# Kernel optimization log

Hardware: AMD Instinct MI355X
Metric: run time of the kernel (lower is better)

The kernel has to match this reference:

```python
import jax, jax.numpy as jnp
import numpy as np

B, T, D = 64, 8192, 128
UNITS = 128

def setup_inputs() -> dict:
    key = jax.random.key(0)
    k1, k2, k3 = jax.random.split(key, 3)
    inputs = jax.random.normal(k1, (B, T, D), dtype=jnp.float32)
    # Dense(units): kernel [D, units], bias [units]
    W_kernel = jax.random.normal(k2, (D, UNITS), dtype=jnp.float32) * (1.0 / np.sqrt(D))
    W_bias = jnp.zeros((UNITS,), dtype=jnp.float32)
    # Dense(1): kernel [units, 1], bias [1]
    V_kernel = jax.random.normal(k3, (UNITS, 1), dtype=jnp.float32) * (1.0 / np.sqrt(UNITS))
    V_bias = jnp.zeros((1,), dtype=jnp.float32)
    return {"inputs": inputs, "W_kernel": W_kernel, "W_bias": W_bias,
            "V_kernel": V_kernel, "V_bias": V_bias}

def reference(inputs, W_kernel, W_bias, V_kernel, V_bias):
    # score: [B, T, units]
    score = jnp.tanh(jnp.einsum('btd,du->btu', inputs, W_kernel) + W_bias)
    # logits: [B, T, 1]; softmax over time axis (axis=1)
    logits = jnp.einsum('btu,uo->bto', score, V_kernel) + V_bias
    attention_weights = jax.nn.softmax(logits, axis=1)
    # weighted sum over time -> [B, D]
    context_vector = jnp.sum(attention_weights * inputs, axis=1)
    return context_vector
```

## Files before the change

### kernel.cpp

```cpp
#include <hip/hip_runtime.h>
#include <hip/hip_bf16.h>

typedef __attribute__((ext_vector_type(8))) short short8;
typedef __attribute__((ext_vector_type(4))) float f32x4;

#define B_SZ 64
#define T_SZ 8192
#define D_SZ 128
#define U_SZ 128
#define T_TILE 64
#define GRID_P 1024
#define TILES_PER_BLK 8
#define P_STRIDE 132
#define WT_LD 136

__device__ __forceinline__ unsigned short f2bf(float f) {
  unsigned int u = __builtin_bit_cast(unsigned int, f);
  u += 0x7fffu + ((u >> 16) & 1u);
  return (unsigned short)(u >> 16);
}

__device__ __forceinline__ float bf2f(unsigned short s) {
  return __builtin_bit_cast(float, (unsigned int)s << 16);
}

__device__ __forceinline__ float fast_tanh(float x) {
  float e = __expf(2.0f * x);
  return 1.0f - 2.0f * __builtin_amdgcn_rcpf(e + 1.0f);
}

template<int CTRL>
__device__ __forceinline__ float dpp_add(float v) {
  int t = __builtin_amdgcn_update_dpp(0, __builtin_bit_cast(int, v),
                                      CTRL, 0xf, 0xf, true);
  return v + __builtin_bit_cast(float, t);
}
__device__ __forceinline__ float row_reduce16(float v) {
  v = dpp_add<0x118>(v);
  v = dpp_add<0x114>(v);
  v = dpp_add<0x112>(v);
  v = dpp_add<0x111>(v);
  return v;
}

__global__ void k_prep(const float* __restrict__ wk, unsigned short* __restrict__ wt) {
  int i = blockIdx.x * 256 + threadIdx.x;
  if (i < D_SZ * U_SZ) {
    int d = i >> 7, u = i & 127;
    wt[u * D_SZ + d] = f2bf(wk[i]);
  }
}

__global__ __launch_bounds__(256) void k_partial(
    const float* __restrict__ x, const unsigned short* __restrict__ wt_g,
    const float* __restrict__ wb, const float* __restrict__ v,
    const float* __restrict__ vb, float* __restrict__ pbuf)
{
  __shared__ unsigned short wt[U_SZ][WT_LD];
  __shared__ float wb_s[U_SZ], v_s[U_SZ];
  __shared__ float logits[T_TILE];
  __shared__ float cpar[4][D_SZ];
  __shared__ float cacc[D_SZ];

  const int tid  = threadIdx.x;
  const int bidx = blockIdx.x;

  for (int i = tid; i < U_SZ * 16; i += 256) {
    int row = i >> 4, c16 = i & 15;
    uint4 val = ((const uint4*)wt_g)[i];
    *(uint4*)&wt[row][c16 * 8] = val;
  }
  if (tid < U_SZ) { wb_s[tid] = wb[tid]; v_s[tid] = v[tid]; cacc[tid] = 0.0f; }
  __syncthreads();

  const int w  = tid >> 6;
  const int l  = tid & 63;
  const int lr = l & 15;
  const int lh = l >> 4;
  const float vbias = vb[0];

  const int b        = bidx >> 4;
  const int row0     = (bidx & 15) * (TILES_PER_BLK * T_TILE);
  const float* xbase = x + ((size_t)b * T_SZ + row0 + w * 16 + lr) * D_SZ + lh * 8;

  float4 pf[8];
#pragma unroll
  for (int kt = 0; kt < 4; ++kt) {
    pf[kt * 2]     = *(const float4*)(xbase + kt * 32);
    pf[kt * 2 + 1] = *(const float4*)(xbase + kt * 32 + 4);
  }
  short8 afrag[4];
#pragma unroll
  for (int kt = 0; kt < 4; ++kt) {
    short8 a;
#pragma unroll
    for (int j = 0; j < 4; ++j) {
      float4 f = pf[kt * 2 + (j >> 1)];
      a[j * 2]     = (short)f2bf(j & 1 ? f.z : f.x);
      a[j * 2 + 1] = (short)f2bf(j & 1 ? f.w : f.y);
    }
    afrag[kt] = a;
  }

  float m_run = -3.0e38f, s_run = 0.0f;

  for (int it = 0; it < TILES_PER_BLK; ++it) {
    if (it + 1 < TILES_PER_BLK) {
      const float* p = xbase + (size_t)(it + 1) * T_TILE * D_SZ;
#pragma unroll
      for (int kt = 0; kt < 4; ++kt) {
        pf[kt * 2]     = *(const float4*)(p + kt * 32);
        pf[kt * 2 + 1] = *(const float4*)(p + kt * 32 + 4);
      }
    }

    float lg[4] = {0.f, 0.f, 0.f, 0.f};
#pragma unroll
    for (int ut = 0; ut < 8; ++ut) {
      f32x4 acc = {0.f, 0.f, 0.f, 0.f};
#pragma unroll
      for (int kt = 0; kt < 4; ++kt) {
        short8 bfrag = *(const short8*)&wt[ut * 16 + lr][kt * 32 + lh * 8];
        acc = __builtin_amdgcn_mfma_f32_16x16x32_bf16(afrag[kt], bfrag, acc, 0, 0, 0);
      }
      const float wbv = wb_s[ut * 16 + lr];
      const float vv  = v_s[ut * 16 + lr];
#pragma unroll
      for (int r = 0; r < 4; ++r)
        lg[r] += fast_tanh(acc[r] + wbv) * vv;
    }
#pragma unroll
    for (int r = 0; r < 4; ++r) lg[r] = row_reduce16(lg[r]);
    if (lr == 15) {
#pragma unroll
      for (int r = 0; r < 4; ++r)
        logits[w * 16 + lh * 4 + r] = lg[r] + vbias;
    }
    __syncthreads();

    float lv = logits[l];
    float mx = lv;
#pragma unroll
    for (int k = 1; k <= 32; k <<= 1) mx = fmaxf(mx, __shfl_xor(mx, k, 64));
    float ss = __expf(lv - mx);
#pragma unroll
    for (int k = 1; k <= 32; k <<= 1) ss += __shfl_xor(ss, k, 64);
    const float pr = __expf(logits[w * 16 + lr] - mx);

#pragma unroll
    for (int kt = 0; kt < 4; ++kt) {
      float csum[8];
#pragma unroll
      for (int j = 0; j < 8; ++j)
        csum[j] = row_reduce16(pr * bf2f((unsigned short)afrag[kt][j]));
      if (lr == 15) {
        f32x4 v0 = {csum[0], csum[1], csum[2], csum[3]};
        f32x4 v1 = {csum[4], csum[5], csum[6], csum[7]};
        *(f32x4*)&cpar[w][kt * 32 + lh * 8]     = v0;
        *(f32x4*)&cpar[w][kt * 32 + lh * 8 + 4] = v1;
      }
    }
    __syncthreads();

    const float m_new = fmaxf(m_run, mx);
    const float e_old = __expf(m_run - m_new);
    const float e_t   = __expf(mx - m_new);
    if (tid < D_SZ) {
      float ct = cpar[0][tid] + cpar[1][tid] + cpar[2][tid] + cpar[3][tid];
      cacc[tid] = cacc[tid] * e_old + ct * e_t;
    }
    s_run = s_run * e_old + ss * e_t;
    m_run = m_new;

    if (it + 1 < TILES_PER_BLK) {
#pragma unroll
      for (int kt = 0; kt < 4; ++kt) {
        short8 a;
#pragma unroll
        for (int j = 0; j < 4; ++j) {
          float4 f = pf[kt * 2 + (j >> 1)];
          a[j * 2]     = (short)f2bf(j & 1 ? f.z : f.x);
          a[j * 2 + 1] = (short)f2bf(j & 1 ? f.w : f.y);
        }
        afrag[kt] = a;
      }
    }
  }

  float* pb = pbuf + (size_t)bidx * P_STRIDE;
  if (tid < 128)       pb[tid] = cacc[tid];
  else if (tid == 128) pb[128] = m_run;
  else if (tid == 129) pb[129] = s_run;
}

__global__ __launch_bounds__(128) void k_combine(const float* __restrict__ pbuf,
                                                 float* __restrict__ out)
{
  const int b = blockIdx.x, tid = threadIdx.x;
  __shared__ float sm[16], sden[16];
  const float* base = pbuf + (size_t)b * 16 * P_STRIDE;

  if (tid < 16) {
    sm[tid]   = base[tid * P_STRIDE + 128];
    sden[tid] = base[tid * P_STRIDE + 129];
  }
  __syncthreads();

  float mx = -3.0e38f;
#pragma unroll
  for (int i = 0; i < 16; ++i) mx = fmaxf(mx, sm[i]);
  float den = 0.0f, c = 0.0f;
#pragma unroll
  for (int i = 0; i < 16; ++i) {
    float e = __expf(sm[i] - mx);
    den += sden[i] * e;
    c = fmaf(base[(size_t)i * P_STRIDE + tid], e, c);
  }
  out[b * D_SZ + tid] = c / den;
}

extern "C" void kernel_launch(void* const* d_in, const int* in_sizes, int n_in,
                              void* d_out, int out_size, void* d_ws, size_t ws_size,
                              hipStream_t stream) {
  const float* x  = (const float*)d_in[0];
  const float* wk = (const float*)d_in[1];
  const float* wb = (const float*)d_in[2];
  const float* vk = (const float*)d_in[3];
  const float* vb = (const float*)d_in[4];
  float* out = (float*)d_out;

  unsigned short* wt = (unsigned short*)d_ws;
  float* pbuf = (float*)((char*)d_ws + 32768);

  k_prep<<<64, 256, 0, stream>>>(wk, wt);
  k_partial<<<GRID_P, 256, 0, stream>>>(x, wt, wb, vk, vb, pbuf);
  k_combine<<<B_SZ, 128, 0, stream>>>(pbuf, out);
}
```

Before: 71.63 us.

## Keep per-wave online softmax state and merge waves once at the end

Each wave now runs its own online softmax (running max, sum, and a 32-float context accumulator in registers) over its 16 rows per tile. This removes the two block-wide __syncthreads and the shared-memory partial reduction that ran every tile. The four waves' partial results are merged only once after the loop, rescaled to a block-wide max. The cost is more live registers per thread, and it relies on a wave's own LDS writes to logits being visible to that wave without a barrier.

```diff
diff --git a/kernel.cpp b/kernel.cpp
--- a/kernel.cpp
+++ b/kernel.cpp
@@ -43,6 +43,20 @@
   return v;
 }
 
+__device__ __forceinline__ void cvt_tile(const float4 pf[8], short8 afrag[4]) {
+#pragma unroll
+  for (int kt = 0; kt < 4; ++kt) {
+    short8 a;
+#pragma unroll
+    for (int j = 0; j < 4; ++j) {
+      float4 f = pf[kt * 2 + (j >> 1)];
+      a[j * 2]     = (short)f2bf(j & 1 ? f.z : f.x);
+      a[j * 2 + 1] = (short)f2bf(j & 1 ? f.w : f.y);
+    }
+    afrag[kt] = a;
+  }
+}
+
 __global__ void k_prep(const float* __restrict__ wk, unsigned short* __restrict__ wt) {
   int i = blockIdx.x * 256 + threadIdx.x;
   if (i < D_SZ * U_SZ) {
@@ -58,9 +72,9 @@
 {
   __shared__ unsigned short wt[U_SZ][WT_LD];
   __shared__ float wb_s[U_SZ], v_s[U_SZ];
-  __shared__ float logits[T_TILE];
-  __shared__ float cpar[4][D_SZ];
-  __shared__ float cacc[D_SZ];
+  __shared__ float logits[4][16];
+  __shared__ float fin[4][D_SZ];
+  __shared__ float fm[4], fs[4];
 
   const int tid  = threadIdx.x;
   const int bidx = blockIdx.x;
@@ -70,7 +84,7 @@
     uint4 val = ((const uint4*)wt_g)[i];
     *(uint4*)&wt[row][c16 * 8] = val;
   }
-  if (tid < U_SZ) { wb_s[tid] = wb[tid]; v_s[tid] = v[tid]; cacc[tid] = 0.0f; }
+  if (tid < U_SZ) { wb_s[tid] = wb[tid]; v_s[tid] = v[tid]; }
   __syncthreads();
 
   const int w  = tid >> 6;
@@ -90,19 +104,14 @@
     pf[kt * 2 + 1] = *(const float4*)(xbase + kt * 32 + 4);
   }
   short8 afrag[4];
-#pragma unroll
-  for (int kt = 0; kt < 4; ++kt) {
-    short8 a;
-#pragma unroll
-    for (int j = 0; j < 4; ++j) {
-      float4 f = pf[kt * 2 + (j >> 1)];
-      a[j * 2]     = (short)f2bf(j & 1 ? f.z : f.x);
-      a[j * 2 + 1] = (short)f2bf(j & 1 ? f.w : f.y);
-    }
-    afrag[kt] = a;
-  }
+  cvt_tile(pf, afrag);
 
   float m_run = -3.0e38f, s_run = 0.0f;
+  float rc[4][8];
+#pragma unroll
+  for (int kt = 0; kt < 4; ++kt)
+#pragma unroll
+    for (int j = 0; j < 8; ++j) rc[kt][j] = 0.0f;
 
   for (int it = 0; it < TILES_PER_BLK; ++it) {
     if (it + 1 < TILES_PER_BLK) {
@@ -134,63 +143,59 @@
     if (lr == 15) {
 #pragma unroll
       for (int r = 0; r < 4; ++r)
-        logits[w * 16 + lh * 4 + r] = lg[r] + vbias;
-    }
-    __syncthreads();
-
-    float lv = logits[l];
+        logits[w][lh * 4 + r] = lg[r] + vbias;
+    }
+
+    float lv = logits[w][lr];
     float mx = lv;
 #pragma unroll
-    for (int k = 1; k <= 32; k <<= 1) mx = fmaxf(mx, __shfl_xor(mx, k, 64));
-    float ss = __expf(lv - mx);
-#pragma unroll
-    for (int k = 1; k <= 32; k <<= 1) ss += __shfl_xor(ss, k, 64);
-    const float pr = __expf(logits[w * 16 + lr] - mx);
-
-#pragma unroll
-    for (int kt = 0; kt < 4; ++kt) {
-      float csum[8];
-#pragma unroll
-      for (int j = 0; j < 8; ++j)
-        csum[j] = row_reduce16(pr * bf2f((unsigned short)afrag[kt][j]));
-      if (lr == 15) {
-        f32x4 v0 = {csum[0], csum[1], csum[2], csum[3]};
-        f32x4 v1 = {csum[4], csum[5], csum[6], csum[7]};
-        *(f32x4*)&cpar[w][kt * 32 + lh * 8]     = v0;
-        *(f32x4*)&cpar[w][kt * 32 + lh * 8 + 4] = v1;
-      }
-    }
-    __syncthreads();
-
+    for (int k = 1; k <= 8; k <<= 1) mx = fmaxf(mx, __shfl_xor(mx, k, 64));
     const float m_new = fmaxf(m_run, mx);
     const float e_old = __expf(m_run - m_new);
-    const float e_t   = __expf(mx - m_new);
-    if (tid < D_SZ) {
-      float ct = cpar[0][tid] + cpar[1][tid] + cpar[2][tid] + cpar[3][tid];
-      cacc[tid] = cacc[tid] * e_old + ct * e_t;
-    }
-    s_run = s_run * e_old + ss * e_t;
+    const float pr    = __expf(lv - m_new);
+    float ss = pr;
+#pragma unroll
+    for (int k = 1; k <= 8; k <<= 1) ss += __shfl_xor(ss, k, 64);
+    s_run = s_run * e_old + ss;
     m_run = m_new;
 
-    if (it + 1 < TILES_PER_BLK) {
-#pragma unroll
-      for (int kt = 0; kt < 4; ++kt) {
-        short8 a;
-#pragma unroll
-        for (int j = 0; j < 4; ++j) {
-          float4 f = pf[kt * 2 + (j >> 1)];
-          a[j * 2]     = (short)f2bf(j & 1 ? f.z : f.x);
-          a[j * 2 + 1] = (short)f2bf(j & 1 ? f.w : f.y);
-        }
-        afrag[kt] = a;
+#pragma unroll
+    for (int kt = 0; kt < 4; ++kt) {
+#pragma unroll
+      for (int j = 0; j < 8; ++j) {
+        float cs = row_reduce16(pr * bf2f((unsigned short)afrag[kt][j]));
+        rc[kt][j] = fmaf(rc[kt][j], e_old, cs);
       }
     }
-  }
+
+    if (it + 1 < TILES_PER_BLK) cvt_tile(pf, afrag);
+  }
+
+  if (l == 0) { fm[w] = m_run; fs[w] = s_run; }
+  __syncthreads();
+  const float m_blk = fmaxf(fmaxf(fm[0], fm[1]), fmaxf(fm[2], fm[3]));
+  const float e_w   = __expf(m_run - m_blk);
+  if (lr == 15) {
+#pragma unroll
+    for (int kt = 0; kt < 4; ++kt) {
+      f32x4 v0 = {rc[kt][0] * e_w, rc[kt][1] * e_w, rc[kt][2] * e_w, rc[kt][3] * e_w};
+      f32x4 v1 = {rc[kt][4] * e_w, rc[kt][5] * e_w, rc[kt][6] * e_w, rc[kt][7] * e_w};
+      *(f32x4*)&fin[w][kt * 32 + lh * 8]     = v0;
+      *(f32x4*)&fin[w][kt * 32 + lh * 8 + 4] = v1;
+    }
+  }
+  __syncthreads();
 
   float* pb = pbuf + (size_t)bidx * P_STRIDE;
-  if (tid < 128)       pb[tid] = cacc[tid];
-  else if (tid == 128) pb[128] = m_run;
-  else if (tid == 129) pb[129] = s_run;
+  if (tid < 128) {
+    pb[tid] = fin[0][tid] + fin[1][tid] + fin[2][tid] + fin[3][tid];
+  } else if (tid == 128) {
+    pb[128] = m_blk;
+  } else if (tid == 129) {
+    float sb = fs[0] * __expf(fm[0] - m_blk) + fs[1] * __expf(fm[1] - m_blk)
+             + fs[2] * __expf(fm[2] - m_blk) + fs[3] * __expf(fm[3] - m_blk);
+    pb[129] = sb;
+  }
 }
 
 __global__ __launch_bounds__(128) void k_combine(const float* __restrict__ pbuf,
```

Result: slower. 88.32 us (+23.3%).
